# Optimization experiments

Hardware: AMD Instinct MI355X
Metric: run time of the kernel (lower is better)

## Reference

```python
import jax, jax.numpy as jnp
import numpy as np

LENGTH = 512
Q = 2 * LENGTH + 3  # num_states = 2*length + 3
ALPHA = 26          # amino-acid alphabet size
BATCH = 256
T = 512


def setup_inputs() -> dict:
    key = jax.random.key(0)
    k1, k2, k3, k4 = jax.random.split(key, 4)
    x = jax.random.randint(k1, (BATCH, T), 0, ALPHA, dtype=jnp.int32)
    A_logits = jax.random.normal(k2, (Q, Q), dtype=jnp.float32)
    B_logits = jax.random.normal(k3, (Q, ALPHA), dtype=jnp.float32)
    init_logits = jax.random.normal(k4, (Q,), dtype=jnp.float32)
    return {"x": x, "A_logits": A_logits, "B_logits": B_logits, "init_logits": init_logits}


def reference(x, A_logits, B_logits, init_logits):
    # Build stochastic matrices (as emitter/transitioner do from their kernels).
    A = jax.nn.softmax(A_logits, axis=-1)        # (q, q) row-stochastic transitions
    B = jax.nn.softmax(B_logits, axis=-1)        # (q, alpha) emission distributions
    init = jax.nn.softmax(init_logits)           # (q,) initial distribution

    # Precompute per-position emission probs: E[b, t, :] = B[:, x[b, t]]
    E = B.T[x]                                   # (B, T, q)

    # First step (self.init branch): forward = E0 * initial distribution
    f0 = E[:, 0] * init[None, :]                 # (B, q)
    S0 = jnp.sum(f0, axis=-1, keepdims=True)     # (B, 1)
    ll0 = jnp.log(S0)
    f0 = f0 / S0

    def step(carry, Et):
        f, ll = carry
        fwd = Et * (f @ A)                       # emit * transition  (B, q)
        S = jnp.sum(fwd, axis=-1, keepdims=True)
        ll = ll + jnp.log(S)
        fwd = fwd / S
        return (fwd, ll), fwd

    (_, loglik), fwd_seq = jax.lax.scan(step, (f0, ll0), jnp.swapaxes(E[:, 1:], 0, 1))
    # fwd_seq: (T-1, B, q) -> full (B, T, q) with first step prepended
    forward = jnp.swapaxes(jnp.concatenate([f0[None], fwd_seq], axis=0), 0, 1)
    return forward, loglik
```

## Files before the change

### kernel.cpp

```cpp
#include <hip/hip_runtime.h>
#include <stdint.h>


#define Q     1027
#define TT    512
#define ALPH  26
#define KCH   33
#define NTILE 65
#define NCHK  (KCH*64)
#define GIMG  (NCHK*16)
#define NCL   16
#define WPC   16
#define MB    16

typedef short  short8  __attribute__((ext_vector_type(8)));
typedef float  floatx4 __attribute__((ext_vector_type(4)));
typedef int    intx4   __attribute__((ext_vector_type(4)));

static constexpr size_t al512(size_t x) { return (x + 511) & ~size_t(511); }
static constexpr size_t OFF_APACK = 0;
static constexpr size_t SZ_APACK  = (size_t)NTILE * KCH * 64 * 16;
static constexpr size_t OFF_BSOFT = al512(OFF_APACK + SZ_APACK);
static constexpr size_t SZ_BSOFT  = (size_t)Q * ALPH * 4;
static constexpr size_t OFF_INIT  = al512(OFF_BSOFT + SZ_BSOFT);
static constexpr size_t OFF_AMAX  = al512(OFF_INIT + Q * 4);
static constexpr size_t OFF_AINV  = al512(OFF_AMAX + Q * 4);
static constexpr size_t OFF_GEX   = al512(OFF_AINV + Q * 4);
static constexpr size_t SZ_GEX    = (size_t)NCL * 2 * GIMG;
static constexpr size_t OFF_FLAGS = al512(OFF_GEX + SZ_GEX);
static constexpr size_t SZ_FLAGS  = (size_t)NCL * WPC * 4;
static constexpr size_t OFF_SPART = al512(OFF_FLAGS + SZ_FLAGS);
static constexpr size_t SZ_SPART  = (size_t)NCL * 2 * WPC * MB * 4;
static constexpr size_t WS_NEED   = OFF_SPART + SZ_SPART;
static constexpr size_t FWDSZ     = (size_t)256 * TT * Q;

__device__ __forceinline__ uint32_t f2bf(float f) {
  uint32_t u = __float_as_uint(f);
  return (u + 0x7fffu + ((u >> 16) & 1u)) >> 16;
}


__global__ void k_zero(char* __restrict__ ws) {
  const size_t n = (WS_NEED - OFF_GEX) / 16;
  intx4* p = (intx4*)(ws + OFF_GEX);
  for (size_t i = (size_t)blockIdx.x * 256 + threadIdx.x; i < n; i += (size_t)72 * 256)
    p[i] = intx4{0, 0, 0, 0};
}

__global__ void k_astats(const float* __restrict__ A, char* __restrict__ ws) {
  const int r = blockIdx.x, tid = threadIdx.x;
  const float* row = A + (size_t)r * Q;
  __shared__ float red[4], red2[4];
  float mx = -3.0e38f;
  for (int i = tid; i < Q; i += 256) mx = fmaxf(mx, row[i]);
#pragma unroll
  for (int d = 1; d < 64; d <<= 1) mx = fmaxf(mx, __shfl_xor(mx, d));
  if ((tid & 63) == 0) red[tid >> 6] = mx;
  __syncthreads();
  mx = fmaxf(fmaxf(red[0], red[1]), fmaxf(red[2], red[3]));
  float s = 0.f;
  for (int i = tid; i < Q; i += 256) s += expf(row[i] - mx);
#pragma unroll
  for (int d = 1; d < 64; d <<= 1) s += __shfl_xor(s, d);
  if ((tid & 63) == 0) red2[tid >> 6] = s;
  __syncthreads();
  s = red2[0] + red2[1] + red2[2] + red2[3];
  if (tid == 0) {
    *(float*)(ws + OFF_AMAX + (size_t)r * 4) = mx;
    *(float*)(ws + OFF_AINV + (size_t)r * 4) = 1.0f / s;
  }
}

__global__ void k_bsoft(const float* __restrict__ Bl, char* __restrict__ ws) {
  const int r = blockIdx.x, l = threadIdx.x;
  float v = (l < ALPH) ? Bl[(size_t)r * ALPH + l] : -3.0e38f;
  float mx = v;
#pragma unroll
  for (int d = 1; d < 64; d <<= 1) mx = fmaxf(mx, __shfl_xor(mx, d));
  float e = (l < ALPH) ? expf(v - mx) : 0.f;
  float s = e;
#pragma unroll
  for (int d = 1; d < 64; d <<= 1) s += __shfl_xor(s, d);
  if (l < ALPH) *(float*)(ws + OFF_BSOFT + ((size_t)r * ALPH + l) * 4) = e / s;
}

__global__ void k_isoft(const float* __restrict__ il, char* __restrict__ ws) {
  const int tid = threadIdx.x;
  __shared__ float red[4], red2[4];
  float mx = -3.0e38f;
  for (int i = tid; i < Q; i += 256) mx = fmaxf(mx, il[i]);
#pragma unroll
  for (int d = 1; d < 64; d <<= 1) mx = fmaxf(mx, __shfl_xor(mx, d));
  if ((tid & 63) == 0) red[tid >> 6] = mx;
  __syncthreads();
  mx = fmaxf(fmaxf(red[0], red[1]), fmaxf(red[2], red[3]));
  float s = 0.f;
  for (int i = tid; i < Q; i += 256) s += expf(il[i] - mx);
#pragma unroll
  for (int d = 1; d < 64; d <<= 1) s += __shfl_xor(s, d);
  if ((tid & 63) == 0) red2[tid >> 6] = s;
  __syncthreads();
  s = red2[0] + red2[1] + red2[2] + red2[3];
  const float inv = 1.0f / s;
  for (int i = tid; i < Q; i += 256)
    *(float*)(ws + OFF_INIT + (size_t)i * 4) = expf(il[i] - mx) * inv;
}

__global__ void k_repack(const float* __restrict__ A, char* __restrict__ ws) {
  const int b = blockIdx.x;
  const int nt = b % NTILE, kc = b / NTILE;
  const int lane = threadIdx.x;
  const int q = nt * 16 + (lane & 15);
  const int kb = kc * 32 + (lane >> 4) * 8;
  union { short8 v; unsigned short u[8]; } pk;
#pragma unroll
  for (int e = 0; e < 8; ++e) {
    const int k = kb + e;
    float val = 0.f;
    if (k < Q && q < Q) {
      const float mxk = *(const float*)(ws + OFF_AMAX + (size_t)k * 4);
      const float ivk = *(const float*)(ws + OFF_AINV + (size_t)k * 4);
      val = expf(A[(size_t)k * Q + q] - mxk) * ivk;
    }
    pk.u[e] = (unsigned short)f2bf(val);
  }
  *(short8*)(ws + OFF_APACK + (((size_t)nt * KCH + kc) * 64 + lane) * 16) = pk.v;
}


__global__ __launch_bounds__(256) void k_main(const int* __restrict__ xin,
                                              char* __restrict__ ws,
                                              float* __restrict__ out) {
  const int bid = blockIdx.x;
  const int c = bid & 15, j = bid >> 4;
  const int tid = threadIdx.x;
  const int lane = tid & 63, w = tid >> 6;
  const int cL = lane & 15, g4 = lane >> 4;
  const bool jx = (j == 15), two = (jx && w == 3);
  const int tg = 4 * j + w;
  const uint64_t wsu = (uint64_t)(uintptr_t)ws;

  __shared__ intx4   g_lds[NCHK];
  __shared__ uint8_t x_lds[MB * TT];
  __shared__ float   B_lds[5][16][ALPH];
  __shared__ float   init_lds[5][16];
  __shared__ float   Sp_lds[4][16];
  __shared__ float   accx_lds[4][64][4];

  for (int idx = tid; idx < MB * TT; idx += 256)
    x_lds[idx] = (uint8_t)xin[(size_t)(c * MB) * TT + idx];
  for (int idx = tid; idx < 5 * 16 * ALPH; idx += 256) {
    const int tl = idx / (16 * ALPH), rem = idx % (16 * ALPH);
    const int cc = rem / ALPH, a = rem % ALPH;
    const int grow = (tl < 4 ? 64 * j + tl * 16 : 1024) + cc;
    B_lds[tl][cc][a] = (grow < Q) ? *(const float*)(ws + OFF_BSOFT + ((size_t)grow * ALPH + a) * 4) : 0.f;
  }
  for (int idx = tid; idx < 5 * 16; idx += 256) {
    const int tl = idx / 16, cc = idx % 16;
    const int grow = (tl < 4 ? 64 * j + tl * 16 : 1024) + cc;
    init_lds[tl][cc] = (grow < Q) ? *(const float*)(ws + OFF_INIT + (size_t)grow * 4) : 0.f;
  }

  short8 af0[KCH];
#pragma unroll
  for (int kc = 0; kc < KCH; ++kc)
    af0[kc] = *(const short8*)(ws + OFF_APACK + (((size_t)tg * KCH + kc) * 64 + lane) * 16);
  short8 af64[9];
  if (jx) {
#pragma unroll
    for (int i = 0; i < 9; ++i) {
      if (i < 8 || w == 3) {
        const int kc = w * 8 + i;
        af64[i] = *(const short8*)(ws + OFF_APACK + (((size_t)64 * KCH + kc) * 64 + lane) * 16);
      }
    }
  }
  __syncthreads();

  float up0[4], up1[4] = {0.f, 0.f, 0.f, 0.f};

#define POST_STEP(TCUR)                                                                   \
  do {                                                                                    \
    const int par_ = (TCUR) & 1;                                                          \
    const uint64_t gb_ = wsu + OFF_GEX + (size_t)(c * 2 + par_) * GIMG;                   \
    const uint64_t b0_ = gb_ + (size_t)((tg >> 1) * 1024 + ((tg & 1) * 2 + (cL >> 3)) * 256 \
                         + g4 * 64 + (cL & 7) * 2);                                       \
    float tmp_[4];                                                                        \
    _Pragma("unroll") for (int r = 0; r < 4; ++r) {                                       \
      uint32_t v0_ = f2bf(up0[r]);                                                        \
      asm volatile("global_store_short %0, %1, off sc0 sc1" ::                            \
                   "v"(b0_ + (size_t)(r * 16)), "v"(v0_) : "memory");                     \
      tmp_[r] = up0[r];                                                                   \
      if (two) {                                                                          \
        const uint64_t bx_ = gb_ + (size_t)(32 * 1024 + (cL >> 3) * 256 + g4 * 64 +       \
                             (cL & 7) * 2);                                               \
        uint32_t v1_ = f2bf(up1[r]);                                                      \
        asm volatile("global_store_short %0, %1, off sc0 sc1" ::                          \
                     "v"(bx_ + (size_t)(r * 16)), "v"(v1_) : "memory");                   \
        tmp_[r] += up1[r];                                                                \
      }                                                                                   \
    }                                                                                     \
    _Pragma("unroll") for (int r = 0; r < 4; ++r) {                                       \
      _Pragma("unroll") for (int d = 1; d < 16; d <<= 1) tmp_[r] += __shfl_xor(tmp_[r], d); \
    }                                                                                     \
    if (cL == 0) {                                                                        \
      _Pragma("unroll") for (int r = 0; r < 4; ++r) Sp_lds[w][g4 * 4 + r] = tmp_[r];      \
    }                                                                                     \
    asm volatile("s_waitcnt vmcnt(0)" ::: "memory");                                      \
    __syncthreads();                                                                      \
    if (w == 0) {                                                                         \
      if (lane < 16) {                                                                    \
        float sw_ = Sp_lds[0][lane] + Sp_lds[1][lane] + Sp_lds[2][lane] + Sp_lds[3][lane];\
        uint64_t sa_ = wsu + OFF_SPART + (size_t)(((c * 2 + par_) * WPC + j) * MB + lane) * 4; \
        asm volatile("global_store_dword %0, %1, off sc0 sc1\n\ts_waitcnt vmcnt(0)" ::    \
                     "v"(sa_), "v"(sw_) : "memory");                                      \
      }                                                                                   \
      if (lane == 0) {                                                                    \
        uint64_t fa_ = wsu + OFF_FLAGS + (size_t)(c * WPC + j) * 4;                       \
        int fv_ = (TCUR) + 1;                                                             \
        asm volatile("global_store_dword %0, %1, off sc0 sc1" :: "v"(fa_), "v"(fv_)       \
                     : "memory");                                                         \
      }                                                                                   \
    }                                                                                     \
  } while (0)

#define WAIT_FLAGS(TGT)                                                                   \
  do {                                                                                    \
    if (w == 0) {                                                                         \
      const uint64_t fa_ = wsu + OFF_FLAGS + (size_t)(c * WPC + cL) * 4;                  \
      for (;;) {                                                                          \
        int f_;                                                                           \
        asm volatile("global_load_dword %0, %1, off sc0 sc1\n\ts_waitcnt vmcnt(0)"        \
                     : "=v"(f_) : "v"(fa_) : "memory");                                   \
        if (__all(f_ >= (TGT))) break;                                                    \
        __builtin_amdgcn_s_sleep(2);                                                      \
      }                                                                                   \
    }                                                                                     \
    __syncthreads();                                                                      \
  } while (0)

#define SPART_BLOCK(PARP, SVAR)                                                           \
  float SVAR;                                                                             \
  do {                                                                                    \
    const uint64_t sb_ = wsu + OFF_SPART + (size_t)((c * 2 + (PARP)) * WPC) * MB * 4;     \
    float p0_, p1_, p2_, p3_;                                                             \
    uint64_t a0_ = sb_ + (size_t)((g4 + 0) * MB + cL) * 4;                                \
    uint64_t a1_ = sb_ + (size_t)((g4 + 4) * MB + cL) * 4;                                \
    uint64_t a2_ = sb_ + (size_t)((g4 + 8) * MB + cL) * 4;                                \
    uint64_t a3_ = sb_ + (size_t)((g4 + 12) * MB + cL) * 4;                               \
    asm volatile("global_load_dword %0, %4, off sc0 sc1\n\t"                              \
                 "global_load_dword %1, %5, off sc0 sc1\n\t"                              \
                 "global_load_dword %2, %6, off sc0 sc1\n\t"                              \
                 "global_load_dword %3, %7, off sc0 sc1\n\t"                              \
                 "s_waitcnt vmcnt(0)"                                                     \
                 : "=v"(p0_), "=v"(p1_), "=v"(p2_), "=v"(p3_)                             \
                 : "v"(a0_), "v"(a1_), "v"(a2_), "v"(a3_) : "memory");                    \
    SVAR = p0_ + p1_ + p2_ + p3_;                                                         \
    SVAR += __shfl_xor(SVAR, 16);                                                         \
    SVAR += __shfl_xor(SVAR, 32);                                                         \
  } while (0)

#pragma unroll
  for (int r = 0; r < 4; ++r) {
    const int m = g4 * 4 + r;
    const int xm = x_lds[m * TT + 0];
    up0[r] = B_lds[w][cL][xm] * init_lds[w][cL];
    if (two) up1[r] = B_lds[4][cL][xm] * init_lds[4][cL];
  }
  POST_STEP(0);

  float llacc = 0.f;

  for (int t = 1; t < TT; ++t) {
    const int parp = (t - 1) & 1;

    WAIT_FLAGS(t);

    const uint64_t gbp = wsu + OFF_GEX + (size_t)(c * 2 + parp) * GIMG;
    intx4 sgv[8], tl4;
#pragma unroll
    for (int i = 0; i < 8; ++i) {
      uint64_t a = gbp + (size_t)((i * 256 + tid) * 16);
      asm volatile("global_load_dwordx4 %0, %1, off sc0 sc1" : "=v"(sgv[i]) : "v"(a) : "memory");
    }
    const bool has9 = (tid < 64);
    if (has9) {
      uint64_t a = gbp + (size_t)((2048 + tid) * 16);
      asm volatile("global_load_dwordx4 %0, %1, off sc0 sc1" : "=v"(tl4) : "v"(a) : "memory");
    }

    SPART_BLOCK(parp, s);

#pragma unroll
    for (int i = 0; i < 8; ++i) g_lds[i * 256 + tid] = sgv[i];
    if (has9) g_lds[2048 + tid] = tl4;

    float invS[4];
#pragma unroll
    for (int r = 0; r < 4; ++r) invS[r] = 1.0f / __shfl(s, g4 * 4 + r);

#pragma unroll
    for (int r = 0; r < 4; ++r) {
      const int m = g4 * 4 + r;
      const size_t ob = ((size_t)(c * MB + m) * TT + (t - 1)) * Q;
      __builtin_nontemporal_store(up0[r] * invS[r], out + ob + tg * 16 + cL);
      if (two && cL < 3)
        __builtin_nontemporal_store(up1[r] * invS[r], out + ob + 1024 + cL);
    }
    __syncthreads();

    floatx4 a0v = {0, 0, 0, 0}, a1v = {0, 0, 0, 0}, a64v = {0, 0, 0, 0};
#pragma unroll
    for (int kc = 0; kc < KCH; ++kc) {
      short8 gf = *(const short8*)&g_lds[kc * 64 + lane];
      if (kc & 1) a1v = __builtin_amdgcn_mfma_f32_16x16x32_bf16(gf, af0[kc], a1v, 0, 0, 0);
      else        a0v = __builtin_amdgcn_mfma_f32_16x16x32_bf16(gf, af0[kc], a0v, 0, 0, 0);
    }
    float r1v[4];
    if (jx) {
#pragma unroll
      for (int i = 0; i < 9; ++i) {
        if (i < 8 || w == 3) {
          const int kc = w * 8 + i;
          short8 gf = *(const short8*)&g_lds[kc * 64 + lane];
          a64v = __builtin_amdgcn_mfma_f32_16x16x32_bf16(gf, af64[i], a64v, 0, 0, 0);
        }
      }
#pragma unroll
      for (int r = 0; r < 4; ++r) accx_lds[w][lane][r] = a64v[r];
      __syncthreads();
      if (two) {
#pragma unroll
        for (int r = 0; r < 4; ++r)
          r1v[r] = accx_lds[0][lane][r] + accx_lds[1][lane][r] +
                   accx_lds[2][lane][r] + accx_lds[3][lane][r];
      }
    }

#pragma unroll
    for (int r = 0; r < 4; ++r) {
      const int m = g4 * 4 + r;
      const int xm = x_lds[m * TT + t];
      up0[r] = (a0v[r] + a1v[r]) * B_lds[w][cL][xm] * invS[r];
      if (two) up1[r] = r1v[r] * B_lds[4][cL][xm] * invS[r];
    }

    POST_STEP(t);
    if (j == 0 && w == 0) llacc += logf(s);
  }

  WAIT_FLAGS(TT);
  {
    SPART_BLOCK((TT - 1) & 1, s);
    if (j == 0 && w == 0) llacc += logf(s);
    float invS[4];
#pragma unroll
    for (int r = 0; r < 4; ++r) invS[r] = 1.0f / __shfl(s, g4 * 4 + r);
#pragma unroll
    for (int r = 0; r < 4; ++r) {
      const int m = g4 * 4 + r;
      const size_t ob = ((size_t)(c * MB + m) * TT + (TT - 1)) * Q;
      __builtin_nontemporal_store(up0[r] * invS[r], out + ob + tg * 16 + cL);
      if (two && cL < 3)
        __builtin_nontemporal_store(up1[r] * invS[r], out + ob + 1024 + cL);
    }
    if (j == 0 && w == 0 && lane < 16) out[FWDSZ + (size_t)c * MB + lane] = llacc;
  }
}


extern "C" void kernel_launch(void* const* d_in, const int* in_sizes, int n_in,
                              void* d_out, int out_size, void* d_ws, size_t ws_size,
                              hipStream_t stream) {
  const int*   x    = (const int*)d_in[0];
  const float* Alog = (const float*)d_in[1];
  const float* Blog = (const float*)d_in[2];
  const float* ilog = (const float*)d_in[3];
  char*  ws  = (char*)d_ws;
  float* out = (float*)d_out;
  if (ws_size < WS_NEED) return;

  hipLaunchKernelGGL(k_zero,   dim3(72),          dim3(256), 0, stream, ws);
  hipLaunchKernelGGL(k_astats, dim3(Q),           dim3(256), 0, stream, Alog, ws);
  hipLaunchKernelGGL(k_bsoft,  dim3(Q),           dim3(64),  0, stream, Blog, ws);
  hipLaunchKernelGGL(k_isoft,  dim3(1),           dim3(256), 0, stream, ilog, ws);
  hipLaunchKernelGGL(k_repack, dim3(NTILE * KCH), dim3(64),  0, stream, Alog, ws);
  hipLaunchKernelGGL(k_main,   dim3(NCL * WPC),   dim3(256), 0, stream, x, ws, out);
}
```

Before: 2.258 ms.

## Split K across waves, publish per-wave partial sums and flags directly

Each wave now computes a quarter of the K dimension for all four of the block's output tiles and reduces the partials through LDS. This replaces the old layout where each wave ran the full K loop for one tile after staging the gathered vector in LDS. Per-wave row-sum partials and completion flags go straight to global memory, which removes the intra-block barrier and single-wave publish step from the post-step. Output stores for the previous step are deferred until after the flag publish, taking them off the critical path. The trade-off is more flags to poll, an LDS cross-wave reduction on every step, and higher register use for four tiles of A fragments.

```diff
diff --git a/kernel.cpp b/kernel.cpp
--- a/kernel.cpp
+++ b/kernel.cpp
@@ -27,11 +27,11 @@
 static constexpr size_t OFF_AINV  = al512(OFF_AMAX + Q * 4);
 static constexpr size_t OFF_GEX   = al512(OFF_AINV + Q * 4);
 static constexpr size_t SZ_GEX    = (size_t)NCL * 2 * GIMG;
-static constexpr size_t OFF_FLAGS = al512(OFF_GEX + SZ_GEX);
-static constexpr size_t SZ_FLAGS  = (size_t)NCL * WPC * 4;
-static constexpr size_t OFF_SPART = al512(OFF_FLAGS + SZ_FLAGS);
-static constexpr size_t SZ_SPART  = (size_t)NCL * 2 * WPC * MB * 4;
-static constexpr size_t WS_NEED   = OFF_SPART + SZ_SPART;
+static constexpr size_t OFF_SP    = al512(OFF_GEX + SZ_GEX);
+static constexpr size_t SZ_SP     = (size_t)NCL * 2 * 64 * MB * 4;
+static constexpr size_t OFF_FLAGS = al512(OFF_SP + SZ_SP);
+static constexpr size_t SZ_FLAGS  = (size_t)NCL * 64 * 4;
+static constexpr size_t WS_NEED   = OFF_FLAGS + SZ_FLAGS;
 static constexpr size_t FWDSZ     = (size_t)256 * TT * Q;
 
 __device__ __forceinline__ uint32_t f2bf(float f) {
@@ -43,7 +43,7 @@
 __global__ void k_zero(char* __restrict__ ws) {
   const size_t n = (WS_NEED - OFF_GEX) / 16;
   intx4* p = (intx4*)(ws + OFF_GEX);
-  for (size_t i = (size_t)blockIdx.x * 256 + threadIdx.x; i < n; i += (size_t)72 * 256)
+  for (size_t i = (size_t)blockIdx.x * 256 + threadIdx.x; i < n; i += (size_t)80 * 256)
     p[i] = intx4{0, 0, 0, 0};
 }
 
@@ -128,24 +128,23 @@
 }
 
 
-__global__ __launch_bounds__(256) void k_main(const int* __restrict__ xin,
-                                              char* __restrict__ ws,
-                                              float* __restrict__ out) {
+__global__ __launch_bounds__(256, 1) void k_main(const int* __restrict__ xin,
+                                                 char* __restrict__ ws,
+                                                 float* __restrict__ out) {
   const int bid = blockIdx.x;
   const int c = bid & 15, j = bid >> 4;
   const int tid = threadIdx.x;
   const int lane = tid & 63, w = tid >> 6;
   const int cL = lane & 15, g4 = lane >> 4;
+  const int tg = 4 * j + w;
   const bool jx = (j == 15), two = (jx && w == 3);
-  const int tg = 4 * j + w;
   const uint64_t wsu = (uint64_t)(uintptr_t)ws;
 
-  __shared__ intx4   g_lds[NCHK];
+  __shared__ floatx4 accx[4][5][64];
   __shared__ uint8_t x_lds[MB * TT];
   __shared__ float   B_lds[5][16][ALPH];
   __shared__ float   init_lds[5][16];
-  __shared__ float   Sp_lds[4][16];
-  __shared__ float   accx_lds[4][64][4];
+  __shared__ float   SpW[4][16];
 
   for (int idx = tid; idx < MB * TT; idx += 256)
     x_lds[idx] = (uint8_t)xin[(size_t)(c * MB) * TT + idx];
@@ -161,23 +160,27 @@
     init_lds[tl][cc] = (grow < Q) ? *(const float*)(ws + OFF_INIT + (size_t)grow * 4) : 0.f;
   }
 
-  short8 af0[KCH];
-#pragma unroll
-  for (int kc = 0; kc < KCH; ++kc)
-    af0[kc] = *(const short8*)(ws + OFF_APACK + (((size_t)tg * KCH + kc) * 64 + lane) * 16);
-  short8 af64[9];
+  short8 af[4][9];
+#pragma unroll
+  for (int tt = 0; tt < 4; ++tt)
+#pragma unroll
+    for (int i = 0; i < 9; ++i)
+      if (i < 8 || w == 0)
+        af[tt][i] = *(const short8*)(ws + OFF_APACK +
+                      (((size_t)(4 * j + tt) * KCH + (4 * i + w)) * 64 + lane) * 16);
+  short8 afx[9];
   if (jx) {
 #pragma unroll
-    for (int i = 0; i < 9; ++i) {
-      if (i < 8 || w == 3) {
-        const int kc = w * 8 + i;
-        af64[i] = *(const short8*)(ws + OFF_APACK + (((size_t)64 * KCH + kc) * 64 + lane) * 16);
-      }
-    }
-  }
-  __syncthreads();
-
-  float up0[4], up1[4] = {0.f, 0.f, 0.f, 0.f};
+    for (int i = 0; i < 9; ++i)
+      if (i < 8 || w == 0)
+        afx[i] = *(const short8*)(ws + OFF_APACK +
+                      (((size_t)64 * KCH + (4 * i + w)) * 64 + lane) * 16);
+  }
+  __syncthreads();
+
+  float up0[4], upx[4] = {0.f, 0.f, 0.f, 0.f};
+  float uold[4], uxold[4] = {0.f, 0.f, 0.f, 0.f};
+  float llacc = 0.f;
 
 #define POST_STEP(TCUR)                                                                   \
   do {                                                                                    \
@@ -185,49 +188,46 @@
     const uint64_t gb_ = wsu + OFF_GEX + (size_t)(c * 2 + par_) * GIMG;                   \
     const uint64_t b0_ = gb_ + (size_t)((tg >> 1) * 1024 + ((tg & 1) * 2 + (cL >> 3)) * 256 \
                          + g4 * 64 + (cL & 7) * 2);                                       \
-    float tmp_[4];                                                                        \
+    float t0_ = up0[0], t1_ = up0[1], t2_ = up0[2], t3_ = up0[3];                         \
     _Pragma("unroll") for (int r = 0; r < 4; ++r) {                                       \
       uint32_t v0_ = f2bf(up0[r]);                                                        \
       asm volatile("global_store_short %0, %1, off sc0 sc1" ::                            \
                    "v"(b0_ + (size_t)(r * 16)), "v"(v0_) : "memory");                     \
-      tmp_[r] = up0[r];                                                                   \
-      if (two) {                                                                          \
-        const uint64_t bx_ = gb_ + (size_t)(32 * 1024 + (cL >> 3) * 256 + g4 * 64 +       \
-                             (cL & 7) * 2);                                               \
-        uint32_t v1_ = f2bf(up1[r]);                                                      \
+    }                                                                                     \
+    if (two) {                                                                            \
+      const uint64_t bx_ = gb_ + (size_t)(32 * 1024 + (cL >> 3) * 256 + g4 * 64 +         \
+                           (cL & 7) * 2);                                                 \
+      _Pragma("unroll") for (int r = 0; r < 4; ++r) {                                     \
+        uint32_t v1_ = f2bf(upx[r]);                                                      \
         asm volatile("global_store_short %0, %1, off sc0 sc1" ::                          \
                      "v"(bx_ + (size_t)(r * 16)), "v"(v1_) : "memory");                   \
-        tmp_[r] += up1[r];                                                                \
       }                                                                                   \
-    }                                                                                     \
-    _Pragma("unroll") for (int r = 0; r < 4; ++r) {                                       \
-      _Pragma("unroll") for (int d = 1; d < 16; d <<= 1) tmp_[r] += __shfl_xor(tmp_[r], d); \
+      t0_ += upx[0]; t1_ += upx[1]; t2_ += upx[2]; t3_ += upx[3];                         \
+    }                                                                                     \
+    _Pragma("unroll") for (int d = 1; d < 16; d <<= 1) {                                  \
+      t0_ += __shfl_xor(t0_, d); t1_ += __shfl_xor(t1_, d);                               \
+      t2_ += __shfl_xor(t2_, d); t3_ += __shfl_xor(t3_, d);                               \
     }                                                                                     \
     if (cL == 0) {                                                                        \
-      _Pragma("unroll") for (int r = 0; r < 4; ++r) Sp_lds[w][g4 * 4 + r] = tmp_[r];      \
+      floatx4 sv_; sv_[0] = t0_; sv_[1] = t1_; sv_[2] = t2_; sv_[3] = t3_;                \
+      uint64_t sa_ = wsu + OFF_SP + (size_t)(c * 2 + par_) * 4096 +                       \
+                     (size_t)(tg * 64 + g4 * 16);                                         \
+      asm volatile("global_store_dwordx4 %0, %1, off sc0 sc1" :: "v"(sa_), "v"(sv_)       \
+                   : "memory");                                                           \
     }                                                                                     \
     asm volatile("s_waitcnt vmcnt(0)" ::: "memory");                                      \
-    __syncthreads();                                                                      \
-    if (w == 0) {                                                                         \
-      if (lane < 16) {                                                                    \
-        float sw_ = Sp_lds[0][lane] + Sp_lds[1][lane] + Sp_lds[2][lane] + Sp_lds[3][lane];\
-        uint64_t sa_ = wsu + OFF_SPART + (size_t)(((c * 2 + par_) * WPC + j) * MB + lane) * 4; \
-        asm volatile("global_store_dword %0, %1, off sc0 sc1\n\ts_waitcnt vmcnt(0)" ::    \
-                     "v"(sa_), "v"(sw_) : "memory");                                      \
-      }                                                                                   \
-      if (lane == 0) {                                                                    \
-        uint64_t fa_ = wsu + OFF_FLAGS + (size_t)(c * WPC + j) * 4;                       \
-        int fv_ = (TCUR) + 1;                                                             \
-        asm volatile("global_store_dword %0, %1, off sc0 sc1" :: "v"(fa_), "v"(fv_)       \
-                     : "memory");                                                         \
-      }                                                                                   \
+    __builtin_amdgcn_sched_barrier(0);                                                    \
+    if (lane == 0) {                                                                      \
+      int fv_ = (TCUR) + 1;                                                               \
+      asm volatile("global_store_dword %0, %1, off sc0 sc1" ::                            \
+                   "v"(wsu + OFF_FLAGS + (size_t)(c * 64 + tg) * 4), "v"(fv_) : "memory");\
     }                                                                                     \
   } while (0)
 
 #define WAIT_FLAGS(TGT)                                                                   \
   do {                                                                                    \
     if (w == 0) {                                                                         \
-      const uint64_t fa_ = wsu + OFF_FLAGS + (size_t)(c * WPC + cL) * 4;                  \
+      const uint64_t fa_ = wsu + OFF_FLAGS + (size_t)(c * 64 + lane) * 4;                 \
       for (;;) {                                                                          \
         int f_;                                                                           \
         asm volatile("global_load_dword %0, %1, off sc0 sc1\n\ts_waitcnt vmcnt(0)"        \
@@ -239,132 +239,137 @@
     __syncthreads();                                                                      \
   } while (0)
 
-#define SPART_BLOCK(PARP, SVAR)                                                           \
-  float SVAR;                                                                             \
-  do {                                                                                    \
-    const uint64_t sb_ = wsu + OFF_SPART + (size_t)((c * 2 + (PARP)) * WPC) * MB * 4;     \
-    float p0_, p1_, p2_, p3_;                                                             \
-    uint64_t a0_ = sb_ + (size_t)((g4 + 0) * MB + cL) * 4;                                \
-    uint64_t a1_ = sb_ + (size_t)((g4 + 4) * MB + cL) * 4;                                \
-    uint64_t a2_ = sb_ + (size_t)((g4 + 8) * MB + cL) * 4;                                \
-    uint64_t a3_ = sb_ + (size_t)((g4 + 12) * MB + cL) * 4;                               \
-    asm volatile("global_load_dword %0, %4, off sc0 sc1\n\t"                              \
-                 "global_load_dword %1, %5, off sc0 sc1\n\t"                              \
-                 "global_load_dword %2, %6, off sc0 sc1\n\t"                              \
-                 "global_load_dword %3, %7, off sc0 sc1\n\t"                              \
-                 "s_waitcnt vmcnt(0)"                                                     \
-                 : "=v"(p0_), "=v"(p1_), "=v"(p2_), "=v"(p3_)                             \
-                 : "v"(a0_), "v"(a1_), "v"(a2_), "v"(a3_) : "memory");                    \
-    SVAR = p0_ + p1_ + p2_ + p3_;                                                         \
-    SVAR += __shfl_xor(SVAR, 16);                                                         \
-    SVAR += __shfl_xor(SVAR, 32);                                                         \
-  } while (0)
-
 #pragma unroll
   for (int r = 0; r < 4; ++r) {
     const int m = g4 * 4 + r;
     const int xm = x_lds[m * TT + 0];
     up0[r] = B_lds[w][cL][xm] * init_lds[w][cL];
-    if (two) up1[r] = B_lds[4][cL][xm] * init_lds[4][cL];
+    uold[r] = up0[r];
+    if (two) { upx[r] = B_lds[4][cL][xm] * init_lds[4][cL]; uxold[r] = upx[r]; }
   }
   POST_STEP(0);
-
-  float llacc = 0.f;
 
   for (int t = 1; t < TT; ++t) {
     const int parp = (t - 1) & 1;
-
     WAIT_FLAGS(t);
 
-    const uint64_t gbp = wsu + OFF_GEX + (size_t)(c * 2 + parp) * GIMG;
-    intx4 sgv[8], tl4;
+    const uint64_t gb = wsu + OFF_GEX + (size_t)(c * 2 + parp) * GIMG;
+    intx4 sg[9], spi;
+#pragma unroll
+    for (int i = 0; i < 8; ++i)
+      asm volatile("global_load_dwordx4 %0, %1, off sc0 sc1"
+                   : "=v"(sg[i]) : "v"(gb + (size_t)((i * 256 + tid) * 16)) : "memory");
+    if (w == 0)
+      asm volatile("global_load_dwordx4 %0, %1, off sc0 sc1"
+                   : "=v"(sg[8]) : "v"(gb + (size_t)((2048 + lane) * 16)) : "memory");
+    asm volatile("global_load_dwordx4 %0, %1, off sc0 sc1"
+                 : "=v"(spi)
+                 : "v"(wsu + OFF_SP + (size_t)(c * 2 + parp) * 4096 + (size_t)tid * 16)
+                 : "memory");
+    asm volatile("s_waitcnt vmcnt(1)" ::: "memory");
+    __builtin_amdgcn_sched_barrier(0);
+
+    floatx4 acc[4] = {{0,0,0,0},{0,0,0,0},{0,0,0,0},{0,0,0,0}};
+    floatx4 acx = {0, 0, 0, 0};
 #pragma unroll
     for (int i = 0; i < 8; ++i) {
-      uint64_t a = gbp + (size_t)((i * 256 + tid) * 16);
-      asm volatile("global_load_dwordx4 %0, %1, off sc0 sc1" : "=v"(sgv[i]) : "v"(a) : "memory");
-    }
-    const bool has9 = (tid < 64);
-    if (has9) {
-      uint64_t a = gbp + (size_t)((2048 + tid) * 16);
-      asm volatile("global_load_dwordx4 %0, %1, off sc0 sc1" : "=v"(tl4) : "v"(a) : "memory");
-    }
-
-    SPART_BLOCK(parp, s);
-
-#pragma unroll
-    for (int i = 0; i < 8; ++i) g_lds[i * 256 + tid] = sgv[i];
-    if (has9) g_lds[2048 + tid] = tl4;
-
-    float invS[4];
-#pragma unroll
-    for (int r = 0; r < 4; ++r) invS[r] = 1.0f / __shfl(s, g4 * 4 + r);
+      const short8 gf = __builtin_bit_cast(short8, sg[i]);
+#pragma unroll
+      for (int tt = 0; tt < 4; ++tt)
+        acc[tt] = __builtin_amdgcn_mfma_f32_16x16x32_bf16(gf, af[tt][i], acc[tt], 0, 0, 0);
+      if (jx) acx = __builtin_amdgcn_mfma_f32_16x16x32_bf16(gf, afx[i], acx, 0, 0, 0);
+    }
+    if (w == 0) {
+      const short8 gf = __builtin_bit_cast(short8, sg[8]);
+#pragma unroll
+      for (int tt = 0; tt < 4; ++tt)
+        acc[tt] = __builtin_amdgcn_mfma_f32_16x16x32_bf16(gf, af[tt][8], acc[tt], 0, 0, 0);
+      if (jx) acx = __builtin_amdgcn_mfma_f32_16x16x32_bf16(gf, afx[8], acx, 0, 0, 0);
+    }
+#pragma unroll
+    for (int tt = 0; tt < 4; ++tt) accx[w][tt][lane] = acc[tt];
+    if (jx) accx[w][4][lane] = acx;
+
+    asm volatile("s_waitcnt vmcnt(0)" ::: "memory");
+    __builtin_amdgcn_sched_barrier(0);
+    floatx4 s4 = __builtin_bit_cast(floatx4, spi);
+#pragma unroll
+    for (int d = 4; d < 64; d <<= 1) {
+#pragma unroll
+      for (int e = 0; e < 4; ++e) s4[e] += __shfl_xor(s4[e], d);
+    }
+    if (lane < 4) *(floatx4*)&SpW[w][lane * 4] = s4;
+    __syncthreads();
+
+    float invS[4], ot0[4], ot1[4];
+    floatx4 rs = accx[0][w][lane] + accx[1][w][lane] + accx[2][w][lane] + accx[3][w][lane];
+    float rx[4];
+    if (two) {
+      floatx4 q = accx[0][4][lane] + accx[1][4][lane] + accx[2][4][lane] + accx[3][4][lane];
+#pragma unroll
+      for (int r = 0; r < 4; ++r) rx[r] = q[r];
+    }
+#pragma unroll
+    for (int r = 0; r < 4; ++r) {
+      const int m = g4 * 4 + r;
+      invS[r] = 1.0f / (SpW[0][m] + SpW[1][m] + SpW[2][m] + SpW[3][m]);
+      ot0[r] = uold[r] * invS[r];
+      if (two) ot1[r] = uxold[r] * invS[r];
+      const int xm = x_lds[m * TT + t];
+      up0[r] = rs[r] * B_lds[w][cL][xm] * invS[r];
+      uold[r] = up0[r];
+      if (two) { upx[r] = rx[r] * B_lds[4][cL][xm] * invS[r]; uxold[r] = upx[r]; }
+    }
+
+    POST_STEP(t);
 
 #pragma unroll
     for (int r = 0; r < 4; ++r) {
       const int m = g4 * 4 + r;
       const size_t ob = ((size_t)(c * MB + m) * TT + (t - 1)) * Q;
-      __builtin_nontemporal_store(up0[r] * invS[r], out + ob + tg * 16 + cL);
+      __builtin_nontemporal_store(ot0[r], out + ob + tg * 16 + cL);
       if (two && cL < 3)
-        __builtin_nontemporal_store(up1[r] * invS[r], out + ob + 1024 + cL);
-    }
+        __builtin_nontemporal_store(ot1[r], out + ob + 1024 + cL);
+    }
+    if (j == 0 && w == 0 && lane < 16)
+      llacc += logf(SpW[0][lane] + SpW[1][lane] + SpW[2][lane] + SpW[3][lane]);
+  }
+
+  WAIT_FLAGS(TT);
+  {
+    const int parp = (TT - 1) & 1;
+    intx4 spi;
+    asm volatile("global_load_dwordx4 %0, %1, off sc0 sc1\n\ts_waitcnt vmcnt(0)"
+                 : "=v"(spi)
+                 : "v"(wsu + OFF_SP + (size_t)(c * 2 + parp) * 4096 + (size_t)tid * 16)
+                 : "memory");
+    __builtin_amdgcn_sched_barrier(0);
+    floatx4 s4 = __builtin_bit_cast(floatx4, spi);
+#pragma unroll
+    for (int d = 4; d < 64; d <<= 1) {
+#pragma unroll
+      for (int e = 0; e < 4; ++e) s4[e] += __shfl_xor(s4[e], d);
+    }
+    if (lane < 4) *(floatx4*)&SpW[w][lane * 4] = s4;
     __syncthreads();
-
-    floatx4 a0v = {0, 0, 0, 0}, a1v = {0, 0, 0, 0}, a64v = {0, 0, 0, 0};
-#pragma unroll
-    for (int kc = 0; kc < KCH; ++kc) {
-      short8 gf = *(const short8*)&g_lds[kc * 64 + lane];
-      if (kc & 1) a1v = __builtin_amdgcn_mfma_f32_16x16x32_bf16(gf, af0[kc], a1v, 0, 0, 0);
-      else        a0v = __builtin_amdgcn_mfma_f32_16x16x32_bf16(gf, af0[kc], a0v, 0, 0, 0);
-    }
-    float r1v[4];
-    if (jx) {
-#pragma unroll
-      for (int i = 0; i < 9; ++i) {
-        if (i < 8 || w == 3) {
-          const int kc = w * 8 + i;
-          short8 gf = *(const short8*)&g_lds[kc * 64 + lane];
-          a64v = __builtin_amdgcn_mfma_f32_16x16x32_bf16(gf, af64[i], a64v, 0, 0, 0);
-        }
-      }
-#pragma unroll
-      for (int r = 0; r < 4; ++r) accx_lds[w][lane][r] = a64v[r];
-      __syncthreads();
-      if (two) {
-#pragma unroll
-        for (int r = 0; r < 4; ++r)
-          r1v[r] = accx_lds[0][lane][r] + accx_lds[1][lane][r] +
-                   accx_lds[2][lane][r] + accx_lds[3][lane][r];
-      }
-    }
-
+    float invS[4];
 #pragma unroll
     for (int r = 0; r < 4; ++r) {
       const int m = g4 * 4 + r;
-      const int xm = x_lds[m * TT + t];
-      up0[r] = (a0v[r] + a1v[r]) * B_lds[w][cL][xm] * invS[r];
-      if (two) up1[r] = r1v[r] * B_lds[4][cL][xm] * invS[r];
-    }
-
-    POST_STEP(t);
-    if (j == 0 && w == 0) llacc += logf(s);
-  }
-
-  WAIT_FLAGS(TT);
-  {
-    SPART_BLOCK((TT - 1) & 1, s);
-    if (j == 0 && w == 0) llacc += logf(s);
-    float invS[4];
-#pragma unroll
-    for (int r = 0; r < 4; ++r) invS[r] = 1.0f / __shfl(s, g4 * 4 + r);
+      invS[r] = 1.0f / (SpW[0][m] + SpW[1][m] + SpW[2][m] + SpW[3][m]);
+    }
 #pragma unroll
     for (int r = 0; r < 4; ++r) {
       const int m = g4 * 4 + r;
       const size_t ob = ((size_t)(c * MB + m) * TT + (TT - 1)) * Q;
       __builtin_nontemporal_store(up0[r] * invS[r], out + ob + tg * 16 + cL);
       if (two && cL < 3)
-        __builtin_nontemporal_store(up1[r] * invS[r], out + ob + 1024 + cL);
-    }
-    if (j == 0 && w == 0 && lane < 16) out[FWDSZ + (size_t)c * MB + lane] = llacc;
+        __builtin_nontemporal_store(upx[r] * invS[r], out + ob + 1024 + cL);
+    }
+    if (j == 0 && w == 0 && lane < 16) {
+      llacc += logf(SpW[0][lane] + SpW[1][lane] + SpW[2][lane] + SpW[3][lane]);
+      out[FWDSZ + (size_t)c * MB + lane] = llacc;
+    }
   }
 }
 
@@ -380,7 +385,7 @@
   float* out = (float*)d_out;
   if (ws_size < WS_NEED) return;
 
-  hipLaunchKernelGGL(k_zero,   dim3(72),          dim3(256), 0, stream, ws);
+  hipLaunchKernelGGL(k_zero,   dim3(80),          dim3(256), 0, stream, ws);
   hipLaunchKernelGGL(k_astats, dim3(Q),           dim3(256), 0, stream, Alog, ws);
   hipLaunchKernelGGL(k_bsoft,  dim3(Q),           dim3(64),  0, stream, Blog, ws);
   hipLaunchKernelGGL(k_isoft,  dim3(1),           dim3(256), 0, stream, ilog, ws);
```

After: 2.152 ms. 4.7% less time.
